# Kernel optimization log

Measured on AMD Instinct MI355X. Metric: run time of the kernel, lower is better.

The kernel has to match this reference:

```python
import jax, jax.numpy as jnp
import numpy as np

N_NODES = 100000
N_EDGES = 3200000
D_IN = 256
D_OUT = 256


def setup_inputs() -> dict:
    key = jax.random.key(0)
    k1, k2, k3, k4, k5 = jax.random.split(key, 5)
    # kaiming-uniform-like init for weight
    bound = float(np.sqrt(6.0 / D_IN))
    weight = jax.random.uniform(k1, (D_IN, D_OUT), dtype=jnp.float32, minval=-bound, maxval=bound)
    bias = jnp.zeros((D_OUT,), dtype=jnp.float32)
    input_feature = jax.random.normal(k2, (N_NODES, D_IN), dtype=jnp.float32)
    # sparse_poly in COO form: (row, col, val), typical normalized graph polynomial values
    edge_row = jax.random.randint(k3, (N_EDGES,), 0, N_NODES, dtype=jnp.int32)
    edge_col = jax.random.randint(k4, (N_EDGES,), 0, N_NODES, dtype=jnp.int32)
    edge_val = jax.random.uniform(k5, (N_EDGES,), dtype=jnp.float32)
    return {
        "input_feature": input_feature,
        "weight": weight,
        "bias": bias,
        "edge_val": edge_val,
        "edge_row": edge_row,
        "edge_col": edge_col,
    }


def reference(input_feature, weight, bias, edge_val, edge_row, edge_col):
    # support = X @ W  -> [N, D_OUT]
    support = input_feature @ weight
    # output = sparse_poly @ support  (COO SpMM):
    # gather source rows, scale by edge values, scatter-add into destination rows
    messages = edge_val[:, None] * support[edge_col]  # [E, D_OUT]
    output = jax.ops.segment_sum(messages, edge_row, num_segments=N_NODES)
    return output + bias
```

## Files before the change

### kernel.cpp

```cpp
#include <hip/hip_runtime.h>

#define D 256
#define GBM 256
#define WT_PITCH 264
#define BSH 9
#define RPB 512
#define NBMAX 256
#define TILE 4096

using bf16x8 = __attribute__((ext_vector_type(8))) short;
using f32x4  = __attribute__((ext_vector_type(4))) float;

static __device__ __forceinline__ unsigned short f2bf(float f) {
    unsigned u = __builtin_bit_cast(unsigned, f);
    return (unsigned short)((u + 0x7fffu + ((u >> 16) & 1u)) >> 16);
}
static __device__ __forceinline__ float as_f(unsigned u) {
    return __builtin_bit_cast(float, u);
}

__global__ void wt_kernel(const float* __restrict__ W, unsigned short* __restrict__ Wt,
                          int* __restrict__ bcounts, int NB) {
    int idx = blockIdx.x * blockDim.x + threadIdx.x;
    int n = idx & 255, k = idx >> 8;
    Wt[n * 256 + k] = f2bf(W[k * 256 + n]);
    if (blockIdx.x == 0 && threadIdx.x < NB) bcounts[threadIdx.x] = 0;
}

__global__ __launch_bounds__(1024) void gemm_mfma(const float* __restrict__ X,
                                                  const unsigned short* __restrict__ Wt,
                                                  unsigned short* __restrict__ S, int N) {
    __shared__ unsigned short wlds[256 * WT_PITCH];

    for (int c = threadIdx.x; c < 8192; c += 1024) {
        int n = c >> 5, kc = c & 31;
        uint4 v = *reinterpret_cast<const uint4*>(Wt + n * 256 + kc * 8);
        *reinterpret_cast<uint4*>(&wlds[n * WT_PITCH + kc * 8]) = v;
    }
    __syncthreads();

    const int lane = threadIdx.x & 63;
    const int wave = threadIdx.x >> 6;
    const int row0 = blockIdx.x * GBM + wave * 16;
    const int l16  = lane & 15;
    const int kgrp = lane >> 4;
    const int arow = min(row0 + l16, N - 1);
    const float* xp = X + (size_t)arow * 256 + kgrp * 8;

    f32x4 acc[16];
#pragma unroll
    for (int i = 0; i < 16; i++) acc[i] = (f32x4)(0.0f);

#pragma unroll
    for (int ks = 0; ks < 8; ks++) {
        float4 a0 = *reinterpret_cast<const float4*>(xp + ks * 32);
        float4 a1 = *reinterpret_cast<const float4*>(xp + ks * 32 + 4);
        bf16x8 af;
        af[0] = (short)f2bf(a0.x); af[1] = (short)f2bf(a0.y);
        af[2] = (short)f2bf(a0.z); af[3] = (short)f2bf(a0.w);
        af[4] = (short)f2bf(a1.x); af[5] = (short)f2bf(a1.y);
        af[6] = (short)f2bf(a1.z); af[7] = (short)f2bf(a1.w);
#pragma unroll
        for (int nt = 0; nt < 16; nt++) {
            bf16x8 bf = *reinterpret_cast<const bf16x8*>(
                &wlds[(nt * 16 + l16) * WT_PITCH + ks * 32 + kgrp * 8]);
            acc[nt] = __builtin_amdgcn_mfma_f32_16x16x32_bf16(af, bf, acc[nt], 0, 0, 0);
        }
    }

#pragma unroll
    for (int nt = 0; nt < 16; nt++) {
#pragma unroll
        for (int j = 0; j < 4; j++) {
            int r = row0 + kgrp * 4 + j;
            if (r < N) S[(size_t)r * 256 + nt * 16 + l16] = f2bf(acc[nt][j]);
        }
    }
}

__global__ __launch_bounds__(256) void bucket_hist(const int* __restrict__ rows,
                                                   int* __restrict__ bcounts,
                                                   int E, int NB) {
    __shared__ int lh[NBMAX];
    for (int i = threadIdx.x; i < NB; i += 256) lh[i] = 0;
    __syncthreads();
    const int stride = gridDim.x * 256;
    for (int e = blockIdx.x * 256 + threadIdx.x; e < E; e += stride)
        atomicAdd(&lh[rows[e] >> BSH], 1);
    __syncthreads();
    for (int i = threadIdx.x; i < NB; i += 256) {
        int v = lh[i];
        if (v) atomicAdd(&bcounts[i], v);
    }
}

__global__ __launch_bounds__(1024) void bscan_kernel(const int* __restrict__ bcounts,
                                                     int* __restrict__ boffs,
                                                     int* __restrict__ bcursor, int NB) {
    __shared__ int wsum[16];
    const int t = threadIdx.x, lane = t & 63, w = t >> 6;
    int x = (t < NB) ? bcounts[t] : 0;
    int s = x;
#pragma unroll
    for (int d = 1; d < 64; d <<= 1) {
        int y = __shfl_up(s, d);
        if (lane >= d) s += y;
    }
    if (lane == 63) wsum[w] = s;
    __syncthreads();
    if (w == 0) {
        int ws = (lane < 16) ? wsum[lane] : 0;
#pragma unroll
        for (int d = 1; d < 16; d <<= 1) {
            int y = __shfl_up(ws, d);
            if (lane >= d) ws += y;
        }
        if (lane < 16) wsum[lane] = ws;
    }
    __syncthreads();
    int excl = (w ? wsum[w - 1] : 0) + s - x;
    if (t < NB) { boffs[t] = excl; bcursor[t] = excl; }
}

__global__ __launch_bounds__(256) void partition_kernel(const int* __restrict__ rows,
                                                        const int* __restrict__ cols,
                                                        const float* __restrict__ vals,
                                                        int* __restrict__ bcursor,
                                                        int2* __restrict__ packed,
                                                        int E, int NB) {
    __shared__ int lh[NBMAX];
    __shared__ int gbase[NBMAX];
    const int t = threadIdx.x;
    const int e0 = blockIdx.x * TILE;

    for (int i = t; i < NB; i += 256) lh[i] = 0;
    __syncthreads();

    int bk[16], rk[16], pc[16], pv[16];
#pragma unroll
    for (int j = 0; j < 16; j++) {
        int idx = e0 + j * 256 + t;
        if (idx < E) {
            int r = rows[idx];
            bk[j] = r >> BSH;
            rk[j] = atomicAdd(&lh[bk[j]], 1);
            pc[j] = ((r & (RPB - 1)) << 17) | cols[idx];
            pv[j] = __float_as_int(vals[idx]);
        } else {
            bk[j] = -1;
        }
    }
    __syncthreads();

    for (int i = t; i < NB; i += 256) {
        int c = lh[i];
        gbase[i] = c ? atomicAdd(&bcursor[i], c) : 0;
    }
    __syncthreads();

#pragma unroll
    for (int j = 0; j < 16; j++) {
        if (bk[j] >= 0) {
            int2 p; p.x = pc[j]; p.y = pv[j];
            packed[(size_t)gbase[bk[j]] + rk[j]] = p;
        }
    }
}

__global__ __launch_bounds__(256) void bucket_scatter(const int2* __restrict__ packed,
                                                      const int* __restrict__ boffs,
                                                      const int* __restrict__ bcounts,
                                                      int* __restrict__ offs,
                                                      int* __restrict__ counts,
                                                      int2* __restrict__ cv, int N) {
    __shared__ int cnt[RPB];
    __shared__ int lofs[RPB];
    __shared__ int wsum[4];
    const int b = blockIdx.x, t = threadIdx.x;
    const int base = boffs[b], nb = bcounts[b];
    const int lane = t & 63, w = t >> 6;

    for (int i = t; i < RPB; i += 256) cnt[i] = 0;
    __syncthreads();
    for (int i = t; i < nb; i += 256)
        atomicAdd(&cnt[((unsigned)packed[base + i].x) >> 17], 1);
    __syncthreads();

    int a0 = cnt[2 * t], a1 = cnt[2 * t + 1];
    int s = a0 + a1;
    int ss = s;
#pragma unroll
    for (int d = 1; d < 64; d <<= 1) {
        int y = __shfl_up(ss, d);
        if (lane >= d) ss += y;
    }
    if (lane == 63) wsum[w] = ss;
    __syncthreads();
    int wex = 0;
    if (w > 0) wex += wsum[0];
    if (w > 1) wex += wsum[1];
    if (w > 2) wex += wsum[2];
    int excl = wex + ss - s;

    const int r0 = b << BSH;
    int r = r0 + 2 * t;
    if (r < N)     { offs[r]     = base + excl;      counts[r]     = a0; }
    if (r + 1 < N) { offs[r + 1] = base + excl + a0; counts[r + 1] = a1; }
    lofs[2 * t]     = excl;
    lofs[2 * t + 1] = excl + a0;
    __syncthreads();

    for (int i = t; i < nb; i += 256) {
        int2 p = packed[base + i];
        int lr = ((unsigned)p.x) >> 17;
        int pos = base + atomicAdd(&lofs[lr], 1);
        int2 o;
        o.x = p.x & 0x1FFFF;
        o.y = p.y;
        cv[pos] = o;
    }
}

__global__ __launch_bounds__(256) void spmm_kernel(const unsigned short* __restrict__ S,
                                                   const int* __restrict__ offs,
                                                   const int* __restrict__ counts,
                                                   const int2* __restrict__ cv,
                                                   const float* __restrict__ bias,
                                                   float* __restrict__ out, int N) {
    const int lane = threadIdx.x & 63;
    const int half = lane >> 5;
    const int l32  = lane & 31;
    const int r = blockIdx.x * 4 + (threadIdx.x >> 6);
    if (r >= N) return;
    const char* Sb = reinterpret_cast<const char*>(S);

    float acc[8] = {0.f, 0.f, 0.f, 0.f, 0.f, 0.f, 0.f, 0.f};
    int i = offs[r];
    const int end = i + counts[r];

#define GPAIR(c0, v0, c1, v1)                                                     \
    {                                                                             \
        int   c = half ? (c1) : (c0);                                             \
        float v = half ? (v1) : (v0);                                             \
        uint4 sv = *reinterpret_cast<const uint4*>(Sb + ((size_t)c << 9) + (l32 << 4)); \
        acc[0] += v * as_f(sv.x << 16);                                           \
        acc[1] += v * as_f(sv.x & 0xffff0000u);                                   \
        acc[2] += v * as_f(sv.y << 16);                                           \
        acc[3] += v * as_f(sv.y & 0xffff0000u);                                   \
        acc[4] += v * as_f(sv.z << 16);                                           \
        acc[5] += v * as_f(sv.z & 0xffff0000u);                                   \
        acc[6] += v * as_f(sv.w << 16);                                           \
        acc[7] += v * as_f(sv.w & 0xffff0000u);                                   \
    }

    for (; i + 7 < end; i += 8) {
        int2 e0 = cv[i],     e1 = cv[i + 1], e2 = cv[i + 2], e3 = cv[i + 3];
        int2 e4 = cv[i + 4], e5 = cv[i + 5], e6 = cv[i + 6], e7 = cv[i + 7];
        GPAIR(e0.x, as_f((unsigned)e0.y), e1.x, as_f((unsigned)e1.y));
        GPAIR(e2.x, as_f((unsigned)e2.y), e3.x, as_f((unsigned)e3.y));
        GPAIR(e4.x, as_f((unsigned)e4.y), e5.x, as_f((unsigned)e5.y));
        GPAIR(e6.x, as_f((unsigned)e6.y), e7.x, as_f((unsigned)e7.y));
    }
    for (; i + 1 < end; i += 2) {
        int2 e0 = cv[i], e1 = cv[i + 1];
        GPAIR(e0.x, as_f((unsigned)e0.y), e1.x, as_f((unsigned)e1.y));
    }
    if (i < end) {
        int2 e0 = cv[i];
        GPAIR(e0.x, as_f((unsigned)e0.y), e0.x, 0.0f);
    }
#undef GPAIR

#pragma unroll
    for (int j = 0; j < 8; j++) acc[j] += __shfl_xor(acc[j], 32);

    float4 bv = reinterpret_cast<const float4*>(bias)[l32 * 2 + half];
    float4 o = { acc[half * 4 + 0] + bv.x, acc[half * 4 + 1] + bv.y,
                 acc[half * 4 + 2] + bv.z, acc[half * 4 + 3] + bv.w };
    reinterpret_cast<float4*>(out)[(size_t)r * 64 + l32 * 2 + half] = o;
}

extern "C" void kernel_launch(void* const* d_in, const int* in_sizes, int n_in,
                              void* d_out, int out_size, void* d_ws, size_t ws_size,
                              hipStream_t stream) {
    const float* X     = (const float*)d_in[0];
    const float* W     = (const float*)d_in[1];
    const float* bias  = (const float*)d_in[2];
    const float* evals = (const float*)d_in[3];
    const int*   erow  = (const int*)d_in[4];
    const int*   ecol  = (const int*)d_in[5];
    float* out = (float*)d_out;

    const int N = in_sizes[0] / D;
    const int E = in_sizes[3];
    const int NB = ((N + RPB - 1) >> BSH);

    char* ws = (char*)d_ws;
    size_t off = 0;
    auto alloc = [&](size_t bytes) {
        void* p = ws + off;
        off += (bytes + 255) & ~(size_t)255;
        return p;
    };
    unsigned short* S  = (unsigned short*)alloc((size_t)N * D * sizeof(unsigned short));
    unsigned short* Wt = (unsigned short*)alloc((size_t)D * D * sizeof(unsigned short));
    int* bcounts = (int*)alloc((size_t)NB * sizeof(int));
    int* boffs   = (int*)alloc((size_t)NB * sizeof(int));
    int* bcursor = (int*)alloc((size_t)NB * sizeof(int));
    int* offs    = (int*)alloc((size_t)N * sizeof(int));
    int* counts  = (int*)alloc((size_t)N * sizeof(int));
    int2* packed = (int2*)alloc((size_t)E * sizeof(int2));
    int2* cv     = (int2*)alloc((size_t)E * sizeof(int2));

    wt_kernel<<<(D * D) / 256, 256, 0, stream>>>(W, Wt, bcounts, NB);
    gemm_mfma<<<(N + GBM - 1) / GBM, 1024, 0, stream>>>(X, Wt, S, N);
    bucket_hist<<<1024, 256, 0, stream>>>(erow, bcounts, E, NB);
    bscan_kernel<<<1, 1024, 0, stream>>>(bcounts, boffs, bcursor, NB);
    partition_kernel<<<(E + TILE - 1) / TILE, 256, 0, stream>>>(erow, ecol, evals, bcursor,
                                                                packed, E, NB);
    bucket_scatter<<<NB, 256, 0, stream>>>(packed, boffs, bcounts, offs, counts, cv, N);
    spmm_kernel<<<(N + 3) / 4, 256, 0, stream>>>(S, offs, counts, cv, bias, out, N);
}
```

Measured before the change: 391.0 us.

## Split SpMM into column slices with per-wave multi-row processing

Replaces the per-row SpMM kernel with one that partitions the 256 output columns into 8 slices of 32, assigning each block 64 rows for one slice. Four edge groups per wave each gather 64-byte slices of bf16 support rows and reduce via shuffles. The intent is to shrink per-edge gather granularity and improve cache locality for the support matrix. In exchange the edge list is read once per slice, rows are processed serially per wave, and fewer lanes do useful stores.

```diff
diff --git a/kernel.cpp b/kernel.cpp
--- a/kernel.cpp
+++ b/kernel.cpp
@@ -221,63 +221,59 @@
     }
 }
 
-__global__ __launch_bounds__(256) void spmm_kernel(const unsigned short* __restrict__ S,
-                                                   const int* __restrict__ offs,
-                                                   const int* __restrict__ counts,
-                                                   const int2* __restrict__ cv,
-                                                   const float* __restrict__ bias,
-                                                   float* __restrict__ out, int N) {
-    const int lane = threadIdx.x & 63;
-    const int half = lane >> 5;
-    const int l32  = lane & 31;
-    const int r = blockIdx.x * 4 + (threadIdx.x >> 6);
-    if (r >= N) return;
-    const char* Sb = reinterpret_cast<const char*>(S);
-
-    float acc[8] = {0.f, 0.f, 0.f, 0.f, 0.f, 0.f, 0.f, 0.f};
-    int i = offs[r];
-    const int end = i + counts[r];
-
-#define GPAIR(c0, v0, c1, v1)                                                     \
-    {                                                                             \
-        int   c = half ? (c1) : (c0);                                             \
-        float v = half ? (v1) : (v0);                                             \
-        uint4 sv = *reinterpret_cast<const uint4*>(Sb + ((size_t)c << 9) + (l32 << 4)); \
-        acc[0] += v * as_f(sv.x << 16);                                           \
-        acc[1] += v * as_f(sv.x & 0xffff0000u);                                   \
-        acc[2] += v * as_f(sv.y << 16);                                           \
-        acc[3] += v * as_f(sv.y & 0xffff0000u);                                   \
-        acc[4] += v * as_f(sv.z << 16);                                           \
-        acc[5] += v * as_f(sv.z & 0xffff0000u);                                   \
-        acc[6] += v * as_f(sv.w << 16);                                           \
-        acc[7] += v * as_f(sv.w & 0xffff0000u);                                   \
-    }
-
-    for (; i + 7 < end; i += 8) {
-        int2 e0 = cv[i],     e1 = cv[i + 1], e2 = cv[i + 2], e3 = cv[i + 3];
-        int2 e4 = cv[i + 4], e5 = cv[i + 5], e6 = cv[i + 6], e7 = cv[i + 7];
-        GPAIR(e0.x, as_f((unsigned)e0.y), e1.x, as_f((unsigned)e1.y));
-        GPAIR(e2.x, as_f((unsigned)e2.y), e3.x, as_f((unsigned)e3.y));
-        GPAIR(e4.x, as_f((unsigned)e4.y), e5.x, as_f((unsigned)e5.y));
-        GPAIR(e6.x, as_f((unsigned)e6.y), e7.x, as_f((unsigned)e7.y));
-    }
-    for (; i + 1 < end; i += 2) {
-        int2 e0 = cv[i], e1 = cv[i + 1];
-        GPAIR(e0.x, as_f((unsigned)e0.y), e1.x, as_f((unsigned)e1.y));
-    }
-    if (i < end) {
-        int2 e0 = cv[i];
-        GPAIR(e0.x, as_f((unsigned)e0.y), e0.x, 0.0f);
-    }
-#undef GPAIR
-
-#pragma unroll
-    for (int j = 0; j < 8; j++) acc[j] += __shfl_xor(acc[j], 32);
-
-    float4 bv = reinterpret_cast<const float4*>(bias)[l32 * 2 + half];
-    float4 o = { acc[half * 4 + 0] + bv.x, acc[half * 4 + 1] + bv.y,
-                 acc[half * 4 + 2] + bv.z, acc[half * 4 + 3] + bv.w };
-    reinterpret_cast<float4*>(out)[(size_t)r * 64 + l32 * 2 + half] = o;
+__global__ __launch_bounds__(256) void spmm_slice(const unsigned short* __restrict__ S,
+                                                  const int* __restrict__ offs,
+                                                  const int* __restrict__ counts,
+                                                  const int2* __restrict__ cv,
+                                                  const float* __restrict__ bias,
+                                                  float* __restrict__ out, int N) {
+    const int lane  = threadIdx.x & 63;
+    const int wave  = threadIdx.x >> 6;
+    const int slice = blockIdx.x & 7;
+    const int rg    = blockIdx.x >> 3;
+    const int q     = lane >> 4;
+    const int c2    = lane & 15;
+    const char* Sb  = reinterpret_cast<const char*>(S);
+    const size_t so = (size_t)(slice << 6) + (c2 << 2);
+
+    const float b0 = bias[slice * 32 + c2 * 2];
+    const float b1 = bias[slice * 32 + c2 * 2 + 1];
+
+    const int rbase = rg * 64 + wave * 16;
+
+#define EDGE(idx)                                                                  \
+    {                                                                              \
+        int2 e = cv[idx];                                                          \
+        unsigned sv = *reinterpret_cast<const unsigned*>(                          \
+            Sb + (((size_t)(unsigned)e.x) << 9) + so);                             \
+        float v = as_f((unsigned)e.y);                                             \
+        a0 += v * as_f(sv << 16);                                                  \
+        a1 += v * as_f(sv & 0xffff0000u);                                          \
+    }
+
+    for (int rr = 0; rr < 16; rr++) {
+        const int r = rbase + rr;
+        if (r >= N) break;
+        int i = offs[r];
+        const int end = i + counts[r];
+        float a0 = 0.f, a1 = 0.f;
+
+        for (; i + 7 < end; i += 8) {
+            EDGE(i + q);
+            EDGE(i + 4 + q);
+        }
+        for (; i + 3 < end; i += 4) EDGE(i + q);
+        if (i + q < end) EDGE(i + q);
+
+        a0 += __shfl_xor(a0, 16); a1 += __shfl_xor(a1, 16);
+        a0 += __shfl_xor(a0, 32); a1 += __shfl_xor(a1, 32);
+
+        if (q == 0) {
+            float2 o = { a0 + b0, a1 + b1 };
+            *reinterpret_cast<float2*>(out + (size_t)r * 256 + slice * 32 + c2 * 2) = o;
+        }
+    }
+#undef EDGE
 }
 
 extern "C" void kernel_launch(void* const* d_in, const int* in_sizes, int n_in,
@@ -319,5 +315,6 @@
     partition_kernel<<<(E + TILE - 1) / TILE, 256, 0, stream>>>(erow, ecol, evals, bcursor,
                                                                 packed, E, NB);
     bucket_scatter<<<NB, 256, 0, stream>>>(packed, boffs, bcounts, offs, counts, cv, N);
-    spmm_kernel<<<(N + 3) / 4, 256, 0, stream>>>(S, offs, counts, cv, bias, out, N);
-}
+    const int nrg = (N + 63) / 64;
+    spmm_slice<<<nrg * 8, 256, 0, stream>>>(S, offs, counts, cv, bias, out, N);
+}
```

Result: slower. 621.5 us (+58.9%).
